# Performance work log

Measured on AMD Instinct MI355X. Metric: run time of the kernel, lower is better.

## Reference

```python
import jax, jax.numpy as jnp
import numpy as np

THRESHOLD = 1.0
B, T, I, H = 128, 512, 512, 1024

def setup_inputs() -> dict:
    key = jax.random.key(0)
    ks = jax.random.split(key, 6)
    s = lambda k, shape, fan: jax.random.normal(k, shape, dtype=jnp.float32) * (1.0 / np.sqrt(fan))
    return {
        "x": jax.random.normal(ks[0], (B, T, I), dtype=jnp.float32),
        "Wi": s(ks[1], (H, I), I),
        "bi": s(ks[2], (H,), I),
        "Wh": s(ks[3], (H, H), H),
        "bh": s(ks[4], (H,), H),
        "h0": jnp.zeros((1, H), dtype=jnp.float32),
    }

def reference(x, Wi, bi, Wh, bh, h0):
    # hidden_init tiled to batch
    hidden = jnp.tile(h0, (x.shape[0], 1))  # [B, H]
    # Precompute input projection for all timesteps in one big GEMM: [B, T, H]
    xin = jnp.einsum('bti,hi->bth', x, Wi) + bi
    xin_t = jnp.swapaxes(xin, 0, 1)  # [T, B, H] for scan

    def step(h, xt):
        pre = h + xt + jnp.dot(h, Wh.T) + bh  # hidden + i2h(x) + h2h(hidden)
        h_new = jnp.minimum(jax.nn.relu(pre), THRESHOLD)
        return h_new, h_new

    hidden, outs = jax.lax.scan(step, hidden, xin_t)
    rnn_out = jnp.swapaxes(outs, 0, 1)  # [B, T, H]
    return rnn_out, hidden
```

## Files before the change

### kernel.cpp

```cpp
#include <hip/hip_runtime.h>
#include <cstddef>

#define B_ 128
#define T_ 512
#define I_ 512
#define H_ 1024
#define TH_ (T_ * H_)
#define PSTR 257
#define LDSN (32 * PSTR)
#define XBN (B_ * H_)

__global__ __launch_bounds__(256) void k_input_gemm(
    const float* __restrict__ A, const float* __restrict__ W,
    const float* __restrict__ bi, float* __restrict__ C)
{
    const int nb = blockIdx.x;
    const int mb = blockIdx.y;
    const int tid = threadIdx.x;
    const int tx = tid & 15;
    const int ty = tid >> 4;

    __shared__ float As[16][132];
    __shared__ float Ws[16][132];

    float acc[8][8];
#pragma unroll
    for (int i = 0; i < 8; ++i)
#pragma unroll
        for (int j = 0; j < 8; ++j) acc[i][j] = 0.f;

    const float* Ab = A + (size_t)mb * 128 * I_;
    const float* Wb = W + (size_t)nb * 128 * I_;

    for (int kt = 0; kt < I_; kt += 16) {
        {
            const int r = tid >> 2;
            const int kq = (tid & 3) * 4;
            float4 v0 = *(const float4*)(Ab + (size_t)r * I_ + kt + kq);
            float4 v1 = *(const float4*)(Ab + (size_t)(r + 64) * I_ + kt + kq);
            As[kq + 0][r] = v0.x; As[kq + 1][r] = v0.y;
            As[kq + 2][r] = v0.z; As[kq + 3][r] = v0.w;
            As[kq + 0][r + 64] = v1.x; As[kq + 1][r + 64] = v1.y;
            As[kq + 2][r + 64] = v1.z; As[kq + 3][r + 64] = v1.w;
            float4 w0 = *(const float4*)(Wb + (size_t)r * I_ + kt + kq);
            float4 w1 = *(const float4*)(Wb + (size_t)(r + 64) * I_ + kt + kq);
            Ws[kq + 0][r] = w0.x; Ws[kq + 1][r] = w0.y;
            Ws[kq + 2][r] = w0.z; Ws[kq + 3][r] = w0.w;
            Ws[kq + 0][r + 64] = w1.x; Ws[kq + 1][r + 64] = w1.y;
            Ws[kq + 2][r + 64] = w1.z; Ws[kq + 3][r + 64] = w1.w;
        }
        __syncthreads();

#pragma unroll
        for (int kk = 0; kk < 16; ++kk) {
            float4 a0 = *(const float4*)&As[kk][ty * 8];
            float4 a1 = *(const float4*)&As[kk][ty * 8 + 4];
            float4 b0 = *(const float4*)&Ws[kk][tx * 8];
            float4 b1 = *(const float4*)&Ws[kk][tx * 8 + 4];
            float av[8] = {a0.x, a0.y, a0.z, a0.w, a1.x, a1.y, a1.z, a1.w};
            float bv[8] = {b0.x, b0.y, b0.z, b0.w, b1.x, b1.y, b1.z, b1.w};
#pragma unroll
            for (int i = 0; i < 8; ++i)
#pragma unroll
                for (int j = 0; j < 8; ++j) acc[i][j] += av[i] * bv[j];
        }
        __syncthreads();
    }

    const int n0 = nb * 128 + tx * 8;
    float4 bv0 = *(const float4*)(bi + n0);
    float4 bv1 = *(const float4*)(bi + n0 + 4);
#pragma unroll
    for (int i = 0; i < 8; ++i) {
        const size_t m = (size_t)mb * 128 + ty * 8 + i;
        float4 c0, c1;
        c0.x = acc[i][0] + bv0.x; c0.y = acc[i][1] + bv0.y;
        c0.z = acc[i][2] + bv0.z; c0.w = acc[i][3] + bv0.w;
        c1.x = acc[i][4] + bv1.x; c1.y = acc[i][5] + bv1.y;
        c1.z = acc[i][6] + bv1.z; c1.w = acc[i][7] + bv1.w;
        *(float4*)(C + m * H_ + n0) = c0;
        *(float4*)(C + m * H_ + n0 + 4) = c1;
    }
}

__device__ __forceinline__ float ofs_of(int t) {
    return 8.0f + 4.0f * (float)((t >> 1) & 1);
}

__global__ __launch_bounds__(256, 2) void k_rnn(
    const float* __restrict__ Wh, const float* __restrict__ bh,
    const float* __restrict__ h0, float* __restrict__ out,
    float* __restrict__ xbuf)
{
    __shared__ float lds[LDSN];

    const int bx = blockIdx.x;
    const int bt = bx & 15;
    const int nt = bx >> 4;
    const int m0 = bt * 8;
    const int n0 = nt * 32;
    const int tid = threadIdx.x;
    const int c = tid & 7;
    const int s = tid >> 3;

    float4 wreg[4][8];
#pragma unroll
    for (int j = 0; j < 4; ++j) {
        const float* wp = Wh + (size_t)(n0 + c * 4 + j) * H_ + s * 4;
#pragma unroll
        for (int jj = 0; jj < 8; ++jj)
            wreg[j][jj] = *(const float4*)(wp + jj * 128);
    }

    const int r  = tid >> 5;
    const int nl = tid & 31;
    const float bh1 = bh[n0 + nl];

    for (int t = 0; t < T_; ++t) {
        const size_t g0 = (size_t)(m0 + r) * TH_ + (size_t)t * H_ + n0 + nl;
        const float xin1 = out[g0];

        if (t == 0) {
#pragma unroll
            for (int i = 0; i < 16; ++i) {
                const int f = i * 256 + tid;
                const int p = f >> 9;
                const int col2 = f & 511;
                const unsigned long long v =
                    *(const unsigned long long*)(h0 + (size_t)col2 * 2);
                *(unsigned long long*)&lds[p * 1024 + col2 * 2] = v;
            }
        } else {
            const unsigned long long* xb = (const unsigned long long*)
                (xbuf + (size_t)((t - 1) & 1) * XBN);
            const float osub = ofs_of(t - 1);
            const float olo = osub - 0.5f;
            const float ohi = osub + 1.5f;

            unsigned long long stg[16];
#pragma unroll
            for (int i = 0; i < 16; ++i) {
                const int f = i * 256 + tid;
                const int p = f >> 9;
                const int col2 = f & 511;
                stg[i] = __hip_atomic_load(&xb[(size_t)(m0 + p) * 512 + col2],
                                           __ATOMIC_RELAXED,
                                           __HIP_MEMORY_SCOPE_SYSTEM);
            }
            for (;;) {
                unsigned bad = 0;
#pragma unroll
                for (int i = 0; i < 16; ++i) {
                    const float lo = __uint_as_float((unsigned)(stg[i] & 0xffffffffull));
                    const float hi = __uint_as_float((unsigned)(stg[i] >> 32));
                    const bool ok = (lo >= olo) & (lo <= ohi) &
                                    (hi >= olo) & (hi <= ohi);
                    if (!ok) bad |= (1u << i);
                }
                if (!bad) break;
#pragma unroll
                for (int i = 0; i < 16; ++i) {
                    if (bad & (1u << i)) {
                        const int f = i * 256 + tid;
                        const int p = f >> 9;
                        const int col2 = f & 511;
                        stg[i] = __hip_atomic_load(&xb[(size_t)(m0 + p) * 512 + col2],
                                                   __ATOMIC_RELAXED,
                                                   __HIP_MEMORY_SCOPE_SYSTEM);
                    }
                }
            }
#pragma unroll
            for (int i = 0; i < 16; ++i) {
                const int f = i * 256 + tid;
                const int p = f >> 9;
                const int col2 = f & 511;
                float lo = __uint_as_float((unsigned)(stg[i] & 0xffffffffull)) - osub;
                float hi = __uint_as_float((unsigned)(stg[i] >> 32)) - osub;
                float2 v; v.x = lo; v.y = hi;
                *(float2*)&lds[p * 1024 + col2 * 2] = v;
            }
        }
        __syncthreads();

        const float hp1 = lds[r * 1024 + n0 + nl];

        float acc[8][4];
#pragma unroll
        for (int m = 0; m < 8; ++m)
#pragma unroll
            for (int j = 0; j < 4; ++j) acc[m][j] = 0.f;

#pragma unroll
        for (int m = 0; m < 8; ++m) {
#pragma unroll
            for (int jj = 0; jj < 8; ++jj) {
                float4 h4 = *(const float4*)&lds[m * 1024 + jj * 128 + s * 4];
#pragma unroll
                for (int j = 0; j < 4; ++j) {
                    acc[m][j] += h4.x * wreg[j][jj].x;
                    acc[m][j] += h4.y * wreg[j][jj].y;
                    acc[m][j] += h4.z * wreg[j][jj].z;
                    acc[m][j] += h4.w * wreg[j][jj].w;
                }
            }
        }
        __syncthreads();

#pragma unroll
        for (int m = 0; m < 8; ++m)
#pragma unroll
            for (int j = 0; j < 4; ++j)
                lds[PSTR * s + m * 32 + c * 4 + j] = acc[m][j];
        __syncthreads();

        float red = 0.f;
#pragma unroll
        for (int g = 0; g < 32; ++g)
            red += lds[PSTR * g + tid];

        const float res = fminf(fmaxf(hp1 + xin1 + red + bh1, 0.f), 1.f);
        out[g0] = res;
        if (t == T_ - 1) {
            out[(size_t)B_ * TH_ + (size_t)(m0 + r) * H_ + n0 + nl] = res;
        } else {
            __hip_atomic_store(
                xbuf + (size_t)(t & 1) * XBN + (size_t)(m0 + r) * H_ + n0 + nl,
                res + ofs_of(t), __ATOMIC_RELAXED, __HIP_MEMORY_SCOPE_SYSTEM);
        }

        __syncthreads();
    }
}

extern "C" void kernel_launch(void* const* d_in, const int* in_sizes, int n_in,
                              void* d_out, int out_size, void* d_ws, size_t ws_size,
                              hipStream_t stream)
{
    const float* x  = (const float*)d_in[0];
    const float* Wi = (const float*)d_in[1];
    const float* bi = (const float*)d_in[2];
    const float* Wh = (const float*)d_in[3];
    const float* bh = (const float*)d_in[4];
    const float* h0 = (const float*)d_in[5];
    float* out = (float*)d_out;
    float* xbuf = (float*)d_ws;

    const size_t need = (size_t)2 * XBN * sizeof(float);
    const size_t zn = ws_size < need ? ws_size : need;
    hipMemsetAsync(d_ws, 0, zn, stream);

    k_input_gemm<<<dim3(8, 512), 256, 0, stream>>>(x, Wi, bi, out);

    k_rnn<<<dim3(512), dim3(256), 0, stream>>>(Wh, bh, h0, out, xbuf);
}
```

Baseline: 5.556 ms.

## Halve RNN block count, split h load to overlap with matvec, vectorize sync I/O

The persistent recurrent kernel now uses 256 blocks, each owning 64 hidden columns with twice as many weight registers per thread. The hidden state for each step is fetched in two halves with inline-asm system-coherent 16-byte loads, so the second half's polling overlaps the first half's matvec. The previous hidden value stays in registers instead of being reread from LDS. Outputs are paired through a lane shuffle into 16-byte nontemporal system stores, and the partial-sum reduction drops from 32 to 16 groups. The cost is higher register pressure at one block per CU and reliance on hand-written cache-control asm and vmcnt waits.

```diff
diff --git a/kernel.cpp b/kernel.cpp
--- a/kernel.cpp
+++ b/kernel.cpp
@@ -6,9 +6,30 @@
 #define I_ 512
 #define H_ 1024
 #define TH_ (T_ * H_)
-#define PSTR 257
-#define LDSN (32 * PSTR)
+#define PSTR3 520
+#define LDSN (16 * PSTR3)
 #define XBN (B_ * H_)
+
+typedef __attribute__((ext_vector_type(4))) float f32x4;
+typedef __attribute__((ext_vector_type(2))) float f32x2;
+
+__device__ __forceinline__ void ldsys16(f32x4& v, const float* p) {
+    asm volatile("global_load_dwordx4 %0, %1, off sc0 sc1"
+                 : "=v"(v) : "v"(p) : "memory");
+}
+__device__ __forceinline__ void stsys16(float* p, f32x4 v) {
+    asm volatile("global_store_dwordx4 %0, %1, off sc0 sc1 nt"
+                 :: "v"(p), "v"(v) : "memory");
+}
+__device__ __forceinline__ void waitvm(int n) {
+    if (n == 0) asm volatile("s_waitcnt vmcnt(0)" ::: "memory");
+    else        asm volatile("s_waitcnt vmcnt(4)" ::: "memory");
+    __builtin_amdgcn_sched_barrier(0);
+}
+
+__device__ __forceinline__ float ofs_of(int t) {
+    return 8.0f + 4.0f * (float)((t >> 1) & 1);
+}
 
 __global__ __launch_bounds__(256) void k_input_gemm(
     const float* __restrict__ A, const float* __restrict__ W,
@@ -83,107 +104,96 @@
     }
 }
 
-__device__ __forceinline__ float ofs_of(int t) {
-    return 8.0f + 4.0f * (float)((t >> 1) & 1);
-}
-
-__global__ __launch_bounds__(256, 2) void k_rnn(
+__global__ __launch_bounds__(256, 1) void k_rnn(
     const float* __restrict__ Wh, const float* __restrict__ bh,
     const float* __restrict__ h0, float* __restrict__ out,
     float* __restrict__ xbuf)
 {
-    __shared__ float lds[LDSN];
+    __shared__ __align__(16) float lds[LDSN];
 
     const int bx = blockIdx.x;
     const int bt = bx & 15;
     const int nt = bx >> 4;
     const int m0 = bt * 8;
-    const int n0 = nt * 32;
+    const int n0 = nt * 64;
     const int tid = threadIdx.x;
-    const int c = tid & 7;
-    const int s = tid >> 3;
-
-    float4 wreg[4][8];
+    const int c = tid & 15;
+    const int s = tid >> 4;
+
+    f32x4 wreg[4][16];
 #pragma unroll
     for (int j = 0; j < 4; ++j) {
         const float* wp = Wh + (size_t)(n0 + c * 4 + j) * H_ + s * 4;
 #pragma unroll
-        for (int jj = 0; jj < 8; ++jj)
-            wreg[j][jj] = *(const float4*)(wp + jj * 128);
+        for (int jj = 0; jj < 16; ++jj)
+            wreg[j][jj] = *(const f32x4*)(wp + jj * 64);
     }
 
     const int r  = tid >> 5;
-    const int nl = tid & 31;
-    const float bh1 = bh[n0 + nl];
+    const int nl = 2 * (tid & 31);
+    const f32x2 bh2 = *(const f32x2*)(bh + n0 + nl);
+    f32x2 hp = *(const f32x2*)(h0 + n0 + nl);
 
     for (int t = 0; t < T_; ++t) {
         const size_t g0 = (size_t)(m0 + r) * TH_ + (size_t)t * H_ + n0 + nl;
-        const float xin1 = out[g0];
-
+        const f32x2 xin2 = *(const f32x2*)(out + g0);
+
+        const float* xb = xbuf + (size_t)((t - 1) & 1) * XBN;
+        const float osub = ofs_of(t - 1);
+        const float olo = osub - 0.5f;
+        const float ohi = osub + 1.5f;
+
+        f32x4 v[8];
         if (t == 0) {
 #pragma unroll
-            for (int i = 0; i < 16; ++i) {
-                const int f = i * 256 + tid;
-                const int p = f >> 9;
-                const int col2 = f & 511;
-                const unsigned long long v =
-                    *(const unsigned long long*)(h0 + (size_t)col2 * 2);
-                *(unsigned long long*)&lds[p * 1024 + col2 * 2] = v;
+            for (int i = 0; i < 4; ++i) {
+                const int F = i * 256 + tid;
+                const int p = F >> 7, c4 = F & 127;
+                const int col = c4 * 4;
+                *(f32x4*)&lds[p * 1024 + col] = *(const f32x4*)(h0 + col);
             }
         } else {
-            const unsigned long long* xb = (const unsigned long long*)
-                (xbuf + (size_t)((t - 1) & 1) * XBN);
-            const float osub = ofs_of(t - 1);
-            const float olo = osub - 0.5f;
-            const float ohi = osub + 1.5f;
-
-            unsigned long long stg[16];
-#pragma unroll
-            for (int i = 0; i < 16; ++i) {
-                const int f = i * 256 + tid;
-                const int p = f >> 9;
-                const int col2 = f & 511;
-                stg[i] = __hip_atomic_load(&xb[(size_t)(m0 + p) * 512 + col2],
-                                           __ATOMIC_RELAXED,
-                                           __HIP_MEMORY_SCOPE_SYSTEM);
-            }
+#pragma unroll
+            for (int q = 0; q < 2; ++q)
+#pragma unroll
+                for (int i = 0; i < 4; ++i) {
+                    const int F = i * 256 + tid;
+                    const int p = F >> 7, c4 = F & 127;
+                    const int col = q * 512 + c4 * 4;
+                    ldsys16(v[q * 4 + i], xb + (size_t)(m0 + p) * H_ + col);
+                }
+            waitvm(4);
             for (;;) {
                 unsigned bad = 0;
 #pragma unroll
-                for (int i = 0; i < 16; ++i) {
-                    const float lo = __uint_as_float((unsigned)(stg[i] & 0xffffffffull));
-                    const float hi = __uint_as_float((unsigned)(stg[i] >> 32));
-                    const bool ok = (lo >= olo) & (lo <= ohi) &
-                                    (hi >= olo) & (hi <= ohi);
+                for (int i = 0; i < 4; ++i) {
+                    const f32x4 q4 = v[i];
+                    const bool ok = (q4.x >= olo) & (q4.x <= ohi) &
+                                    (q4.y >= olo) & (q4.y <= ohi) &
+                                    (q4.z >= olo) & (q4.z <= ohi) &
+                                    (q4.w >= olo) & (q4.w <= ohi);
                     if (!ok) bad |= (1u << i);
                 }
                 if (!bad) break;
 #pragma unroll
-                for (int i = 0; i < 16; ++i) {
+                for (int i = 0; i < 4; ++i)
                     if (bad & (1u << i)) {
-                        const int f = i * 256 + tid;
-                        const int p = f >> 9;
-                        const int col2 = f & 511;
-                        stg[i] = __hip_atomic_load(&xb[(size_t)(m0 + p) * 512 + col2],
-                                                   __ATOMIC_RELAXED,
-                                                   __HIP_MEMORY_SCOPE_SYSTEM);
+                        const int F = i * 256 + tid;
+                        const int p = F >> 7, c4 = F & 127;
+                        ldsys16(v[i], xb + (size_t)(m0 + p) * H_ + c4 * 4);
                     }
-                }
-            }
-#pragma unroll
-            for (int i = 0; i < 16; ++i) {
-                const int f = i * 256 + tid;
-                const int p = f >> 9;
-                const int col2 = f & 511;
-                float lo = __uint_as_float((unsigned)(stg[i] & 0xffffffffull)) - osub;
-                float hi = __uint_as_float((unsigned)(stg[i] >> 32)) - osub;
-                float2 v; v.x = lo; v.y = hi;
-                *(float2*)&lds[p * 1024 + col2 * 2] = v;
-            }
-        }
-        __syncthreads();
-
-        const float hp1 = lds[r * 1024 + n0 + nl];
+                waitvm(0);
+            }
+#pragma unroll
+            for (int i = 0; i < 4; ++i) {
+                const int F = i * 256 + tid;
+                const int p = F >> 7, c4 = F & 127;
+                f32x4 q4 = v[i];
+                q4.x -= osub; q4.y -= osub; q4.z -= osub; q4.w -= osub;
+                *(f32x4*)&lds[p * 1024 + c4 * 4] = q4;
+            }
+        }
+        __syncthreads();
 
         float acc[8][4];
 #pragma unroll
@@ -192,10 +202,10 @@
             for (int j = 0; j < 4; ++j) acc[m][j] = 0.f;
 
 #pragma unroll
-        for (int m = 0; m < 8; ++m) {
+        for (int m = 0; m < 8; ++m)
 #pragma unroll
             for (int jj = 0; jj < 8; ++jj) {
-                float4 h4 = *(const float4*)&lds[m * 1024 + jj * 128 + s * 4];
+                const f32x4 h4 = *(const f32x4*)&lds[m * 1024 + jj * 64 + s * 4];
 #pragma unroll
                 for (int j = 0; j < 4; ++j) {
                     acc[m][j] += h4.x * wreg[j][jj].x;
@@ -204,31 +214,105 @@
                     acc[m][j] += h4.w * wreg[j][jj].w;
                 }
             }
+
+        if (t == 0) {
+#pragma unroll
+            for (int i = 0; i < 4; ++i) {
+                const int F = i * 256 + tid;
+                const int p = F >> 7, c4 = F & 127;
+                const int col = 512 + c4 * 4;
+                *(f32x4*)&lds[p * 1024 + col] = *(const f32x4*)(h0 + col);
+            }
+        } else {
+            waitvm(0);
+            for (;;) {
+                unsigned bad = 0;
+#pragma unroll
+                for (int i = 4; i < 8; ++i) {
+                    const f32x4 q4 = v[i];
+                    const bool ok = (q4.x >= olo) & (q4.x <= ohi) &
+                                    (q4.y >= olo) & (q4.y <= ohi) &
+                                    (q4.z >= olo) & (q4.z <= ohi) &
+                                    (q4.w >= olo) & (q4.w <= ohi);
+                    if (!ok) bad |= (1u << i);
+                }
+                if (!bad) break;
+#pragma unroll
+                for (int i = 4; i < 8; ++i)
+                    if (bad & (1u << i)) {
+                        const int F = (i - 4) * 256 + tid;
+                        const int p = F >> 7, c4 = F & 127;
+                        ldsys16(v[i], xb + (size_t)(m0 + p) * H_ + 512 + c4 * 4);
+                    }
+                waitvm(0);
+            }
+#pragma unroll
+            for (int i = 4; i < 8; ++i) {
+                const int F = (i - 4) * 256 + tid;
+                const int p = F >> 7, c4 = F & 127;
+                f32x4 q4 = v[i];
+                q4.x -= osub; q4.y -= osub; q4.z -= osub; q4.w -= osub;
+                *(f32x4*)&lds[p * 1024 + 512 + c4 * 4] = q4;
+            }
         }
         __syncthreads();
 
 #pragma unroll
         for (int m = 0; m < 8; ++m)
 #pragma unroll
-            for (int j = 0; j < 4; ++j)
-                lds[PSTR * s + m * 32 + c * 4 + j] = acc[m][j];
-        __syncthreads();
-
-        float red = 0.f;
-#pragma unroll
-        for (int g = 0; g < 32; ++g)
-            red += lds[PSTR * g + tid];
-
-        const float res = fminf(fmaxf(hp1 + xin1 + red + bh1, 0.f), 1.f);
-        out[g0] = res;
-        if (t == T_ - 1) {
-            out[(size_t)B_ * TH_ + (size_t)(m0 + r) * H_ + n0 + nl] = res;
-        } else {
-            __hip_atomic_store(
-                xbuf + (size_t)(t & 1) * XBN + (size_t)(m0 + r) * H_ + n0 + nl,
-                res + ofs_of(t), __ATOMIC_RELAXED, __HIP_MEMORY_SCOPE_SYSTEM);
-        }
-
+            for (int jj = 8; jj < 16; ++jj) {
+                const f32x4 h4 = *(const f32x4*)&lds[m * 1024 + jj * 64 + s * 4];
+#pragma unroll
+                for (int j = 0; j < 4; ++j) {
+                    acc[m][j] += h4.x * wreg[j][jj].x;
+                    acc[m][j] += h4.y * wreg[j][jj].y;
+                    acc[m][j] += h4.z * wreg[j][jj].z;
+                    acc[m][j] += h4.w * wreg[j][jj].w;
+                }
+            }
+        __syncthreads();
+
+#pragma unroll
+        for (int m = 0; m < 8; ++m) {
+            f32x4 pv;
+            pv.x = acc[m][0]; pv.y = acc[m][1];
+            pv.z = acc[m][2]; pv.w = acc[m][3];
+            *(f32x4*)&lds[PSTR3 * s + m * 64 + c * 4] = pv;
+        }
+        __syncthreads();
+
+        f32x2 red; red.x = 0.f; red.y = 0.f;
+#pragma unroll
+        for (int g = 0; g < 16; ++g) {
+            const f32x2 p2 = *(const f32x2*)&lds[PSTR3 * g + 2 * tid];
+            red.x += p2.x; red.y += p2.y;
+        }
+
+        f32x2 res;
+        res.x = fminf(fmaxf(hp.x + xin2.x + red.x + bh2.x, 0.f), 1.f);
+        res.y = fminf(fmaxf(hp.y + xin2.y + red.y + bh2.y, 0.f), 1.f);
+        hp = res;
+
+        const unsigned long long mine =
+            __builtin_bit_cast(unsigned long long, res);
+        const unsigned long long part = __shfl_xor(mine, 1, 64);
+        if (!(tid & 1)) {
+            const f32x2 pf = __builtin_bit_cast(f32x2, part);
+            f32x4 quad;
+            quad.x = res.x; quad.y = res.y; quad.z = pf.x; quad.w = pf.y;
+            *(f32x4*)(out + g0) = quad;
+            if (t == T_ - 1) {
+                *(f32x4*)(out + (size_t)B_ * TH_ +
+                          (size_t)(m0 + r) * H_ + n0 + nl) = quad;
+            } else {
+                const float oadd = ofs_of(t);
+                f32x4 qo;
+                qo.x = quad.x + oadd; qo.y = quad.y + oadd;
+                qo.z = quad.z + oadd; qo.w = quad.w + oadd;
+                stsys16(xbuf + (size_t)(t & 1) * XBN +
+                        (size_t)(m0 + r) * H_ + n0 + nl, qo);
+            }
+        }
         __syncthreads();
     }
 }
@@ -252,5 +336,5 @@
 
     k_input_gemm<<<dim3(8, 512), 256, 0, stream>>>(x, Wi, bi, out);
 
-    k_rnn<<<dim3(512), dim3(256), 0, stream>>>(Wh, bh, h0, out, xbuf);
-}
+    k_rnn<<<dim3(256), dim3(256), 0, stream>>>(Wh, bh, h0, out, xbuf);
+}
```

After: 16.63 ms. +199.3%, slower.
